# Optimization experiments

Measured on AMD Instinct MI355X. Metric: run time of the kernel, lower is better.

Reference implementation:

```python
import jax, jax.numpy as jnp
import numpy as np

S, B, C = 56, 32, 1024
T = 48
H = 1024          # hidden_size_decoder (== context_size C)
EMB = 512
RANK = 128
VOCAB = 32000


def setup_inputs() -> dict:
    key = jax.random.key(0)
    ks = jax.random.split(key, 16)
    w = 0.05
    inp = {
        "encoded": jax.random.normal(ks[0], (S, B, C), jnp.float32),
        "encoder_state": jax.random.normal(ks[1], (2, B, H), jnp.float32) * 0.1,
        "tgt_tokens": jax.random.randint(ks[2], (B, T), 0, VOCAB),
        "enc_lens": jax.random.randint(ks[3], (B,), S // 2, S + 1).astype(jnp.int32),
        "tgt_lens": jax.random.randint(ks[4], (B,), T // 2, T + 1).astype(jnp.int32),
        "E": jax.random.normal(ks[5], (VOCAB, RANK), jnp.float32) * w,
        "P": jax.random.normal(ks[6], (RANK, EMB), jnp.float32) * w,
        "W0": jax.random.normal(ks[7], (EMB + C, 4 * H), jnp.float32) * w,
        "U0": jax.random.normal(ks[8], (H, 4 * H), jnp.float32) * w,
        "b0": jnp.zeros((4 * H,), jnp.float32),
        "W1": jax.random.normal(ks[9], (H, 4 * H), jnp.float32) * w,
        "U1": jax.random.normal(ks[10], (H, 4 * H), jnp.float32) * w,
        "b1": jnp.zeros((4 * H,), jnp.float32),
        "Wo": jax.random.normal(ks[11], (H + C, EMB), jnp.float32) * w,
        "bo": jnp.zeros((EMB,), jnp.float32),
    }
    return inp


def _lstm_cell(x, h, c, W, U, b):
    gates = x @ W + h @ U + b                      # [B, 4H]
    i, f, g, o = jnp.split(gates, 4, axis=-1)      # torch LSTMCell gate order
    c_new = jax.nn.sigmoid(f) * c + jax.nn.sigmoid(i) * jnp.tanh(g)
    h_new = jax.nn.sigmoid(o) * jnp.tanh(c_new)
    return h_new, c_new


def reference(encoded, encoder_state, tgt_tokens, enc_lens, tgt_lens,
              E, P, W0, U0, b0, W1, U1, b1, Wo, bo):
    # encoded: [S, B, C] (padded encoder outputs), encoder_state: [L=2, B, H]
    enc_b = jnp.transpose(encoded, (1, 0, 2))                 # [B, S, C]
    enc_mask = jnp.arange(S)[None, :] >= enc_lens[:, None]    # [B, S] True = pad

    # factorized embedding lookup (dropout p=0)
    emb = (E[tgt_tokens] @ P)                                 # [B, T, EMB]
    emb_t = jnp.transpose(emb, (1, 0, 2))[: T - 1]            # [T-1, B, EMB]

    h0 = encoder_state                                        # [2, B, H]
    c0 = jnp.zeros_like(encoder_state)
    ctx0 = jnp.zeros((B, C), encoded.dtype)

    def step(carry, x_emb):
        h, c, ctx = carry
        x = jnp.concatenate([x_emb, ctx], axis=-1)            # [B, EMB+C]
        h0n, c0n = _lstm_cell(x, h[0], c[0], W0, U0, b0)
        h1n, c1n = _lstm_cell(h0n, h[1], c[1], W1, U1, b1)
        query = h1n                                           # no context projection
        scores = jnp.einsum("bsc,bc->bs", enc_b, query)       # [B, S]
        scores = jnp.where(enc_mask, -jnp.inf, scores)
        p_att = jax.nn.softmax(scores, axis=-1)
        ctx_new = jnp.einsum("bs,bsc->bc", p_att, enc_b)      # [B, C]
        return (jnp.stack([h0n, h1n]), jnp.stack([c0n, c1n]), ctx_new), (h1n, ctx_new)

    _, (decs, ctxs) = jax.lax.scan(step, (h0, c0, ctx0), emb_t)  # each [T-1, B, *]

    feats = jnp.concatenate([decs, ctxs], axis=-1)            # [T-1, B, H+C]
    hproj = jnp.tanh(feats @ Wo + bo)                          # [T-1, B, EMB]
    logits = (hproj @ P.T) @ E.T                               # [T-1, B, VOCAB]

    labels = tgt_tokens[:, 1:].T                               # [T-1, B]
    logp = jax.nn.log_softmax(logits, axis=-1)
    nll = -jnp.take_along_axis(logp, labels[..., None], axis=-1)[..., 0]
    valid = jnp.arange(T - 1)[:, None] < (tgt_lens[None, :] - 1)  # step t predicts token t+1
    loss = jnp.sum(jnp.where(valid, nll, 0.0))                 # CrossEntropyLoss(reduction='sum')
    return loss
```

## Files before the change

### kernel.cpp

```cpp
#include <hip/hip_runtime.h>
#include <math.h>

#define S_   56
#define B_   32
#define C_   1024
#define T_   48
#define TS   47
#define H_   1024
#define EMB_ 512
#define RANK_ 128
#define VOCAB_ 32000
#define G4   4096
#define NBLK 256

#define FL_DONE 8192
#define FL_P    8224
#define FL_SIZE 10496

using bf16x8 = __attribute__((ext_vector_type(8))) __bf16;
using f32x4  = __attribute__((ext_vector_type(4))) float;

__device__ __forceinline__ float sigmoidf_(float x){ return 1.0f/(1.0f+expf(-x)); }
__device__ __forceinline__ float b2f(__bf16 x){ return (float)x; }
__device__ __forceinline__ f32x4 z4(){ f32x4 z = {0.f,0.f,0.f,0.f}; return z; }

#define AG __HIP_MEMORY_SCOPE_AGENT
__device__ __forceinline__ void stc_u64(void* p, unsigned long long v){
  __hip_atomic_store((unsigned long long*)p, v, __ATOMIC_RELAXED, AG);
}

struct RedShared {
  float red[4][2][16][18];
};
struct AttnShared {
  union { float hS[1024]; float cred[7][64][8]; } u;
  float sS[64];
  float pS[64];
};
union alignas(16) SharedU { RedShared r; AttnShared a; };

__device__ __forceinline__ void bar_arrive(unsigned* bars, int bi, unsigned e){
  asm volatile("s_waitcnt vmcnt(0)" ::: "memory");
  __syncthreads();
  if (threadIdx.x == 0)
    __hip_atomic_store(bars + (size_t)bi*32, e, __ATOMIC_RELAXED, AG);
}
__device__ __forceinline__ void bar_wait_all(unsigned* bars, int bi, unsigned e){
  if (bi == 255){
    if (threadIdx.x < 256){
      while (__hip_atomic_load(bars + (size_t)threadIdx.x*32, __ATOMIC_RELAXED, AG) < e) {}
    }
    __syncthreads();
    if (threadIdx.x == 0)
      __hip_atomic_store(bars + FL_DONE, e, __ATOMIC_RELAXED, AG);
  } else {
    if (threadIdx.x == 0){
      while (__hip_atomic_load(bars + FL_DONE, __ATOMIC_RELAXED, AG) < e) {}
    }
    __syncthreads();
  }
  asm volatile("" ::: "memory");
}
__device__ __forceinline__ void bar_wait_direct(unsigned* bars, unsigned e){
  if (threadIdx.x < 256){
    while (__hip_atomic_load(bars + (size_t)threadIdx.x*32, __ATOMIC_RELAXED, AG) < e) {}
  }
  __syncthreads();
  asm volatile("" ::: "memory");
}
__device__ __forceinline__ void pflag_wait(unsigned* bars, unsigned t){
  if (threadIdx.x < 64){
    while (__hip_atomic_load(bars + FL_P + (size_t)threadIdx.x*32, __ATOMIC_RELAXED, AG) < t)
      __builtin_amdgcn_s_sleep(2);
  }
  __syncthreads();
  asm volatile("" ::: "memory");
}

__global__ void k_init(const float* __restrict__ es, __bf16* h0bm1, __bf16* fm1,
                       unsigned* bars){
  int i = blockIdx.x*blockDim.x + threadIdx.x;
  if (i < 32*H_){
    int b = i >> 10, j = i & 1023;
    h0bm1[(size_t)b*1024 + j]       = (__bf16)es[i];
    fm1[(size_t)b*2048 + j]         = (__bf16)es[32*H_ + i];
    fm1[(size_t)b*2048 + 1024 + j]  = (__bf16)0.0f;
  }
  if (i < FL_SIZE) bars[i] = 0u;
}

__global__ void k_cvt(const float* __restrict__ src, __bf16* __restrict__ dst, int n){
  int i = (blockIdx.x*blockDim.x + threadIdx.x)*4;
  if (i < n){
    float4 v = *(const float4*)(src + i);
    dst[i+0]=(__bf16)v.x; dst[i+1]=(__bf16)v.y; dst[i+2]=(__bf16)v.z; dst[i+3]=(__bf16)v.w;
  }
}

__global__ void k_embed(const float* __restrict__ E, const float* __restrict__ P,
                        const int* __restrict__ tok, __bf16* __restrict__ embb){
  int blk = blockIdx.x;
  int t = blk >> 5, b = blk & 31, tid = threadIdx.x;
  __shared__ float er[RANK_];
  int tk = tok[b*T_ + t];
  er[tid] = E[(size_t)tk*RANK_ + tid];
  __syncthreads();
  float4 acc = {0.f,0.f,0.f,0.f};
  int e = tid*4;
  for (int r2 = 0; r2 < RANK_; r2++){
    float ev = er[r2];
    float4 p = *(const float4*)(P + (size_t)r2*EMB_ + e);
    acc.x += ev*p.x; acc.y += ev*p.y; acc.z += ev*p.z; acc.w += ev*p.w;
  }
  size_t o = (size_t)blk*EMB_ + e;
  embb[o+0]=(__bf16)acc.x; embb[o+1]=(__bf16)acc.y;
  embb[o+2]=(__bf16)acc.z; embb[o+3]=(__bf16)acc.w;
}

__global__ void k_pack2(const float* __restrict__ W, int K1, const float* __restrict__ U,
                        __bf16* __restrict__ dst, int NCH){
  int ch = blockIdx.x;
  int g  = blockIdx.y >> 2;
  int band = blockIdx.y & 3;
  int tid = threadIdx.x;
  __shared__ __bf16 Tl[32][264];
  {
    int r = tid>>3, cs = tid&7;
    int kk = ch*32 + r;
    const float* src = (kk < K1) ? (W + (size_t)kk*G4 + g*1024 + band*256 + cs*32)
                                 : (U + (size_t)(kk-K1)*G4 + g*1024 + band*256 + cs*32);
    #pragma unroll
    for (int u=0;u<8;u++){
      float4 v = *(const float4*)(src + u*4);
      Tl[r][cs*32+u*4+0]=(__bf16)v.x; Tl[r][cs*32+u*4+1]=(__bf16)v.y;
      Tl[r][cs*32+u*4+2]=(__bf16)v.z; Tl[r][cs*32+u*4+3]=(__bf16)v.w;
    }
  }
  __syncthreads();
  int bil = tid>>2, aq = tid&3;
  int bi = band*64 + bil;
  #pragma unroll
  for (int q=0;q<4;q++){
    __bf16 o8[8];
    #pragma unroll
    for (int i=0;i<8;i++) o8[i] = Tl[aq*8+i][bil*4+q];
    int lane = aq*16 + g*4 + q;
    *(bf16x8*)(dst + (((size_t)bi*NCH + ch)*64 + lane)*8) = *(bf16x8*)o8;
  }
}

__global__ void k_packB(const float* __restrict__ src, __bf16* __restrict__ dst,
                        int K, int N, int tr){
  int kk0 = blockIdx.x*32, j0 = blockIdx.y*16, lane = threadIdx.x;
  int am = lane&15, aq = lane>>4;
  int j = j0 + am;
  __bf16 o8[8];
  #pragma unroll
  for (int i=0;i<8;i++){
    int k = kk0 + aq*8 + i;
    float v = tr ? src[(size_t)j*K + k] : src[(size_t)k*N + j];
    o8[i] = (__bf16)v;
  }
  int NCH = K/32, jt = j0>>4, ch = kk0>>5;
  *(bf16x8*)(dst + (((size_t)jt*NCH + ch)*64 + lane)*8) = *(bf16x8*)o8;
}

template<int NC>
__device__ __forceinline__ void accum(f32x4& acc0, f32x4& acc1,
    const __bf16* __restrict__ abase, int rs, const __bf16* wlds,
    int ch0, int am, int aq, int lane)
{
  const __bf16* a0p = abase + (size_t)am*rs + aq*8;
  const __bf16* a1p = abase + (size_t)(am+16)*rs + aq*8;
  const __bf16* wl  = wlds + (size_t)lane*8;
  #pragma unroll
  for (int c=0;c<NC;c++){
    int ch = ch0 + c;
    bf16x8 a0 = *(const bf16x8*)(a0p + (size_t)ch*32);
    bf16x8 a1 = *(const bf16x8*)(a1p + (size_t)ch*32);
    bf16x8 w  = *(const bf16x8*)(wl  + (size_t)ch*512);
    acc0 = __builtin_amdgcn_mfma_f32_16x16x32_bf16(a0, w, acc0, 0, 0, 0);
    acc1 = __builtin_amdgcn_mfma_f32_16x16x32_bf16(a1, w, acc1, 0, 0, 0);
  }
}

__device__ __forceinline__ void reduce_cell(SharedU& su, const f32x4& acc0, const f32x4& acc1,
    int bi, int tid, const float* __restrict__ bias, float& creg,
    __bf16* __restrict__ hout, int stride)
{
  int kw = tid>>6, lane = tid&63, am = lane&15, aq = lane>>4;
  if (kw >= 4){
    #pragma unroll
    for (int rg=0;rg<4;rg++){
      su.r.red[kw-4][0][aq*4+rg][am] = acc0[rg];
      su.r.red[kw-4][1][aq*4+rg][am] = acc1[rg];
    }
  }
  __syncthreads();
  if (kw < 4){
    #pragma unroll
    for (int rg=0;rg<4;rg++){
      su.r.red[kw][0][aq*4+rg][am] += acc0[rg];
      su.r.red[kw][1][aq*4+rg][am] += acc1[rg];
    }
  }
  __syncthreads();
  if (tid < 128){
    int b = tid>>2, q = tid&3;
    int mt = b>>4, r = b&15;
    float G0=0.f, G1=0.f, G2=0.f, G3=0.f;
    #pragma unroll
    for (int w2=0; w2<4; w2++){
      G0 += su.r.red[w2][mt][r][q];
      G1 += su.r.red[w2][mt][r][4+q];
      G2 += su.r.red[w2][mt][r][8+q];
      G3 += su.r.red[w2][mt][r][12+q];
    }
    int j = bi*4 + q;
    float gi = G0 + bias[j];
    float gf = G1 + bias[1024 + j];
    float gg = G2 + bias[2048 + j];
    float go = G3 + bias[3072 + j];
    float ii = sigmoidf_(gi), ff = sigmoidf_(gf), gv = tanhf(gg), oo = sigmoidf_(go);
    float cv = ff*creg + ii*gv;
    float hv = oo*tanhf(cv);
    creg = cv;
    union { __bf16 h; unsigned short s; } hu; hu.h = (__bf16)hv;
    unsigned h0v = hu.s;
    unsigned h1v = __shfl_down(h0v, 1);
    unsigned h2v = __shfl_down(h0v, 2);
    unsigned h3v = __shfl_down(h0v, 3);
    if (q == 0){
      unsigned long long pk = (unsigned long long)(h0v & 0xffffu)
                            | ((unsigned long long)(h1v & 0xffffu) << 16)
                            | ((unsigned long long)(h2v & 0xffffu) << 32)
                            | ((unsigned long long)(h3v & 0xffffu) << 48);
      stc_u64(hout + (size_t)b*stride + bi*4, pk);
    }
  }
}

__device__ __forceinline__ void attn_block(AttnShared& sa, int b, int chalf, int tid,
    const __bf16* __restrict__ encb, const int* __restrict__ enc_lens,
    __bf16* __restrict__ fbt)
{
  if (tid < 128){
    bf16x8 h8 = *(const bf16x8*)(fbt + (size_t)b*2048 + tid*8);
    #pragma unroll
    for (int u=0;u<8;u++) sa.u.hS[tid*8+u] = b2f(h8[u]);
  }
  __syncthreads();
  int w = tid >> 6, lane = tid & 63;
  for (int s = w; s < S_; s += 8){
    const __bf16* er = encb + ((size_t)s*32 + b)*C_;
    float a = 0.f;
    #pragma unroll
    for (int half = 0; half < 2; half++){
      int k = lane*8 + half*512;
      bf16x8 e8 = *(const bf16x8*)(er + k);
      #pragma unroll
      for (int u=0;u<8;u++) a += b2f(e8[u]) * sa.u.hS[k+u];
    }
    #pragma unroll
    for (int off=32; off>0; off>>=1) a += __shfl_down(a, off);
    if (lane == 0) sa.sS[s] = a;
  }
  __syncthreads();
  if (tid < 64){
    int len = enc_lens[b];
    float sc = (tid < len && tid < S_) ? sa.sS[tid] : -1e30f;
    float m = sc;
    #pragma unroll
    for (int off=32; off>0; off>>=1) m = fmaxf(m, __shfl_xor(m, off));
    float e = expf(sc - m);
    float ssum = e;
    #pragma unroll
    for (int off=32; off>0; off>>=1) ssum += __shfl_xor(ssum, off);
    sa.pS[tid] = e / ssum;
  }
  __syncthreads();
  int cg = tid & 63, sg = tid >> 6;
  float a8[8];
  #pragma unroll
  for (int i=0;i<8;i++) a8[i] = 0.f;
  for (int s = sg; s < S_; s += 8){
    float p = sa.pS[s];
    bf16x8 e8 = *(const bf16x8*)(encb + ((size_t)s*32 + b)*C_ + chalf*512 + cg*8);
    #pragma unroll
    for (int i=0;i<8;i++) a8[i] += p * b2f(e8[i]);
  }
  if (sg > 0){
    #pragma unroll
    for (int i=0;i<8;i++) sa.u.cred[sg-1][cg][i] = a8[i];
  }
  __syncthreads();
  if (sg == 0){
    union { __bf16 bb[8]; unsigned long long u[2]; } cu;
    #pragma unroll
    for (int i=0;i<8;i++){
      float v = a8[i];
      #pragma unroll
      for (int k=0;k<7;k++) v += sa.u.cred[k][cg][i];
      cu.bb[i] = (__bf16)v;
    }
    stc_u64(fbt + (size_t)b*2048 + 1024 + chalf*512 + cg*8,     cu.u[0]);
    stc_u64(fbt + (size_t)b*2048 + 1024 + chalf*512 + cg*8 + 4, cu.u[1]);
  }
}

__global__ __launch_bounds__(512) void k_loop(
    const __bf16* __restrict__ WP0, const __bf16* __restrict__ WP1,
    const float* __restrict__ b0, const float* __restrict__ b1,
    __bf16* __restrict__ h0b,
    __bf16* __restrict__ featsb,
    const __bf16* __restrict__ embb,
    const __bf16* __restrict__ encb, const int* __restrict__ enc_lens,
    unsigned* bars)
{
  __shared__ __bf16 wB0[80*512];
  __shared__ __bf16 wB1[64*512];
  __shared__ SharedU su;
  int bi = blockIdx.x, tid = threadIdx.x;
  int kw = tid>>6, lane = tid&63, am = lane&15, aq = lane>>4;

  {
    const bf16x8* g0 = (const bf16x8*)(WP0 + (size_t)bi*80*512);
    const bf16x8* g1 = (const bf16x8*)(WP1 + (size_t)bi*64*512);
    bf16x8* l0 = (bf16x8*)wB0;
    bf16x8* l1 = (bf16x8*)wB1;
    for (int idx = tid; idx < 80*64; idx += 512) l0[idx] = g0[idx];
    for (int idx = tid; idx < 64*64; idx += 512) l1[idx] = g1[idx];
  }
  __syncthreads();

  float c0r = 0.f, c1r = 0.f;
  f32x4 g00 = z4(), g01 = z4(), g10 = z4(), g11 = z4();

  accum<2>(g00, g01, embb,                 512,  wB0, kw*2,    am, aq, lane);
  accum<4>(g00, g01, h0b - 32768 - 1536,   1024, wB0, 48+kw*4, am, aq, lane);

  unsigned e = 0;
  for (int t = 0; t < TS; t++){
    const __bf16* fprev = featsb + ((size_t)(t-1))*65536;
    __bf16* h0t = h0b + (size_t)t*32768;
    __bf16* ft  = featsb + (size_t)t*65536;

    pflag_wait(bars, (unsigned)t);
    accum<4>(g00, g01, fprev + 512, 2048, wB0, 16+kw*4, am, aq, lane);
    reduce_cell(su, g00, g01, bi, tid, b0, c0r, h0t, 1024);
    g00 = z4(); g01 = z4();
    bar_arrive(bars, bi, ++e);
    accum<4>(g10, g11, fprev - 1024, 2048, wB1, 32+kw*4, am, aq, lane);
    bar_wait_all(bars, bi, e);

    accum<4>(g10, g11, h0t, 1024, wB1, kw*4, am, aq, lane);
    reduce_cell(su, g10, g11, bi, tid, b1, c1r, ft, 2048);
    g10 = z4(); g11 = z4();
    bar_arrive(bars, bi, ++e);
    if (t + 1 < TS){
      accum<2>(g00, g01, embb + (size_t)(t+1)*16384, 512,  wB0, kw*2,    am, aq, lane);
      accum<4>(g00, g01, h0t - 1536,                 1024, wB0, 48+kw*4, am, aq, lane);
    }

    if (bi < 64){
      bar_wait_direct(bars, e);
      attn_block(su.a, bi & 31, bi >> 5, tid, encb, enc_lens, ft);
      asm volatile("s_waitcnt vmcnt(0)" ::: "memory");
      __syncthreads();
      if (tid == 0)
        __hip_atomic_store(bars + FL_P + (size_t)bi*32, (unsigned)(t+1), __ATOMIC_RELAXED, AG);
    }
  }
}

__global__ __launch_bounds__(256) void k_hproj_mfma(
    const __bf16* __restrict__ fb, const __bf16* __restrict__ WoP,
    const float* __restrict__ bo, __bf16* __restrict__ hpb)
{
  int nt = blockIdx.x, jb = blockIdx.y, tid = threadIdx.x;
  int w = tid>>6, lane = tid&63;
  int mt = w&1, jw = w>>1;
  int am = lane&15, aq = lane>>4;
  const __bf16* aRow = fb + ((size_t)(nt*32 + mt*16 + am))*2048 + aq*8;
  int jt = jb*2 + jw;
  const __bf16* bptr = WoP + ((size_t)jt*64)*512 + lane*8;
  f32x4 acc = {0,0,0,0};
  bf16x8 ar0 = *(const bf16x8*)(aRow);
  bf16x8 br0 = *(const bf16x8*)(bptr);
  bf16x8 ar1 = *(const bf16x8*)(aRow + 32);
  bf16x8 br1 = *(const bf16x8*)(bptr + 512);
  for (int ch = 0; ch < 64; ch += 2){
    bf16x8 a0 = ar0, b0 = br0, a1 = ar1, b1 = br1;
    if (ch + 2 < 64){
      ar0 = *(const bf16x8*)(aRow + (ch+2)*32);
      br0 = *(const bf16x8*)(bptr + (size_t)(ch+2)*512);
      ar1 = *(const bf16x8*)(aRow + (ch+3)*32);
      br1 = *(const bf16x8*)(bptr + (size_t)(ch+3)*512);
    }
    acc = __builtin_amdgcn_mfma_f32_16x16x32_bf16(a0, b0, acc, 0, 0, 0);
    acc = __builtin_amdgcn_mfma_f32_16x16x32_bf16(a1, b1, acc, 0, 0, 0);
  }
  int jcol = jb*32 + jw*16 + am;
  float bv = bo[jcol];
  #pragma unroll
  for (int rg=0; rg<4; rg++){
    int m = nt*32 + mt*16 + aq*4 + rg;
    hpb[(size_t)m*512 + jcol] = (__bf16)tanhf(acc[rg] + bv);
  }
}

__global__ __launch_bounds__(256) void k_rproj_mfma(
    const __bf16* __restrict__ hpb, const __bf16* __restrict__ PP,
    __bf16* __restrict__ rb)
{
  int nt = blockIdx.x, jb = blockIdx.y, tid = threadIdx.x;
  int w = tid>>6, lane = tid&63;
  int mt = w&1, jw = w>>1;
  int am = lane&15, aq = lane>>4;
  const __bf16* aRow = hpb + ((size_t)(nt*32 + mt*16 + am))*512 + aq*8;
  int jt = jb*2 + jw;
  const __bf16* bptr = PP + ((size_t)jt*16)*512 + lane*8;
  f32x4 acc = {0,0,0,0};
  #pragma unroll
  for (int ch = 0; ch < 16; ch++){
    bf16x8 a = *(const bf16x8*)(aRow + ch*32);
    bf16x8 b = *(const bf16x8*)(bptr + (size_t)ch*512);
    acc = __builtin_amdgcn_mfma_f32_16x16x32_bf16(a, b, acc, 0, 0, 0);
  }
  int jcol = jb*32 + jw*16 + am;
  #pragma unroll
  for (int rg=0; rg<4; rg++){
    int m = nt*32 + mt*16 + aq*4 + rg;
    rb[(size_t)m*RANK_ + jcol] = (__bf16)acc[rg];
  }
}

__global__ __launch_bounds__(256) void k_vocab2(
    const __bf16* __restrict__ rb, const __bf16* __restrict__ Eb,
    const int* __restrict__ tok,
    float* __restrict__ mpart, float* __restrict__ lpart,
    float* __restrict__ lablog)
{
  int vc = blockIdx.x, tid = threadIdx.x;
  int w = tid>>6, lane = tid&63;
  int am = lane&15, aq = lane>>4;
  int vb = vc*128 + w*32;
  bf16x8 bfr[2][4];
  #pragma unroll
  for (int vt=0; vt<2; vt++)
    #pragma unroll
    for (int ks=0; ks<4; ks++)
      bfr[vt][ks] = *(const bf16x8*)(Eb + ((size_t)(vb + vt*16 + am))*RANK_ + ks*32 + aq*8);

  __shared__ float redM[4][32], redL[4][32];
  for (int nt = 0; nt < TS; nt++){
    f32x4 acc[2][2] = {{{0,0,0,0},{0,0,0,0}},{{0,0,0,0},{0,0,0,0}}};
    #pragma unroll
    for (int mt=0; mt<2; mt++){
      #pragma unroll
      for (int ks=0; ks<4; ks++){
        bf16x8 a = *(const bf16x8*)(rb + ((size_t)(nt*32 + mt*16 + am))*RANK_ + ks*32 + aq*8);
        acc[mt][0] = __builtin_amdgcn_mfma_f32_16x16x32_bf16(a, bfr[0][ks], acc[mt][0], 0,0,0);
        acc[mt][1] = __builtin_amdgcn_mfma_f32_16x16x32_bf16(a, bfr[1][ks], acc[mt][1], 0,0,0);
      }
    }
    #pragma unroll
    for (int mt=0; mt<2; mt++){
      #pragma unroll
      for (int rg=0; rg<4; rg++){
        int row = mt*16 + aq*4 + rg;
        int n = nt*32 + row;
        int lbl = tok[row*T_ + nt + 1];
        float v0 = acc[mt][0][rg], v1 = acc[mt][1][rg];
        if (vb + am == lbl)      lablog[n] = v0;
        if (vb + 16 + am == lbl) lablog[n] = v1;
        float m = fmaxf(v0, v1);
        #pragma unroll
        for (int off=1; off<16; off<<=1) m = fmaxf(m, __shfl_xor(m, off));
        float l = expf(v0 - m) + expf(v1 - m);
        #pragma unroll
        for (int off=1; off<16; off<<=1) l += __shfl_xor(l, off);
        if (am == 0){ redM[w][row] = m; redL[w][row] = l; }
      }
    }
    __syncthreads();
    if (tid < 32){
      float M = fmaxf(fmaxf(redM[0][tid], redM[1][tid]), fmaxf(redM[2][tid], redM[3][tid]));
      float L = 0.f;
      #pragma unroll
      for (int ww=0; ww<4; ww++) L += redL[ww][tid]*expf(redM[ww][tid] - M);
      mpart[(size_t)(nt*32 + tid)*250 + vc] = M;
      lpart[(size_t)(nt*32 + tid)*250 + vc] = L;
    }
    __syncthreads();
  }
}

__global__ void k_loss1(const float* __restrict__ mpart, const float* __restrict__ lpart,
                        const float* __restrict__ lablog, const int* __restrict__ tgt_lens,
                        float* __restrict__ tpart){
  int t = blockIdx.x, tid = threadIdx.x;
  int row = tid >> 3, cq = tid & 7;
  int n = t*32 + row;
  float m = -1e30f;
  for (int c = cq; c < 250; c += 8) m = fmaxf(m, mpart[(size_t)n*250 + c]);
  #pragma unroll
  for (int off=1; off<8; off<<=1) m = fmaxf(m, __shfl_xor(m, off));
  float l = 0.f;
  for (int c = cq; c < 250; c += 8) l += lpart[(size_t)n*250 + c]*expf(mpart[(size_t)n*250 + c] - m);
  #pragma unroll
  for (int off=1; off<8; off<<=1) l += __shfl_xor(l, off);
  __shared__ float red[32];
  if (cq == 0)
    red[row] = (t < tgt_lens[row] - 1) ? (m + logf(l) - lablog[n]) : 0.f;
  __syncthreads();
  if (tid == 0){
    float s = 0.f;
    #pragma unroll
    for (int i=0;i<32;i++) s += red[i];
    tpart[t] = s;
  }
}

__global__ void k_loss2(const float* __restrict__ tpart, float* __restrict__ out){
  int tid = threadIdx.x;
  float v = (tid < TS) ? tpart[tid] : 0.f;
  #pragma unroll
  for (int off=32; off>0; off>>=1) v += __shfl_down(v, off);
  if (tid == 0) out[0] = v;
}

extern "C" void kernel_launch(void* const* d_in, const int* in_sizes, int n_in,
                              void* d_out, int out_size, void* d_ws, size_t ws_size,
                              hipStream_t stream){
  const float* enc      = (const float*)d_in[0];
  const float* es       = (const float*)d_in[1];
  const int*   tok      = (const int*)  d_in[2];
  const int*   enc_lens = (const int*)  d_in[3];
  const int*   tgt_lens = (const int*)  d_in[4];
  const float* E        = (const float*)d_in[5];
  const float* P        = (const float*)d_in[6];
  const float* W0       = (const float*)d_in[7];
  const float* U0       = (const float*)d_in[8];
  const float* b0       = (const float*)d_in[9];
  const float* W1       = (const float*)d_in[10];
  const float* U1       = (const float*)d_in[11];
  const float* b1       = (const float*)d_in[12];
  const float* Wo       = (const float*)d_in[13];
  const float* bo       = (const float*)d_in[14];
  float* out = (float*)d_out;

  float* fb = (float*)d_ws;
  size_t fo = 0;
  float* mpart = fb + fo; fo += (size_t)TS*32*250;
  float* lpart = fb + fo; fo += (size_t)TS*32*250;
  float* lab   = fb + fo; fo += (size_t)TS*32;
  float* tpart = fb + fo; fo += 64;
  unsigned* bars = (unsigned*)(fb + fo); fo += FL_SIZE;
  __bf16* bb = (__bf16*)(fb + fo);
  size_t bo2 = 0;
  __bf16* WP0    = bb + bo2; bo2 += (size_t)4096*2560;
  __bf16* WP1    = bb + bo2; bo2 += (size_t)4096*2048;
  __bf16* encb   = bb + bo2; bo2 += (size_t)S_*32*C_;
  __bf16* embb   = bb + bo2; bo2 += (size_t)TS*32*EMB_;
  __bf16* rbuf   = bb + bo2; bo2 += (size_t)TS*32*RANK_;
  __bf16* WoP    = bb + bo2; bo2 += (size_t)2048*512;
  __bf16* PP     = bb + bo2; bo2 += (size_t)512*128;
  __bf16* featsb0= bb + bo2; bo2 += (size_t)(TS+1)*32*2048;
  __bf16* hpb    = bb + bo2; bo2 += (size_t)TS*32*EMB_;
  __bf16* h0b0   = bb + bo2; bo2 += (size_t)(TS+1)*32*1024;
  __bf16* Eb     = WP0;

  __bf16* featsb = featsb0 + (size_t)32*2048;
  __bf16* h0b    = h0b0 + (size_t)32*1024;

  k_init<<<128, 256, 0, stream>>>(es, h0b0, featsb0, bars);
  k_cvt<<<(S_*32*C_/4 + 255)/256, 256, 0, stream>>>(enc, encb, S_*32*C_);
  k_embed<<<TS*32, 128, 0, stream>>>(E, P, tok, embb);
  k_pack2<<<dim3(80,16), 256, 0, stream>>>(W0, 1536, U0, WP0, 80);
  k_pack2<<<dim3(64,16), 256, 0, stream>>>(W1, 1024, U1, WP1, 64);
  k_packB<<<dim3(64,32), 64, 0, stream>>>(Wo, WoP, 2048, 512, 0);
  k_packB<<<dim3(16,8), 64, 0, stream>>>(P, PP, 512, 128, 1);

  k_loop<<<NBLK, 512, 0, stream>>>(WP0, WP1, b0, b1, h0b, featsb,
                                   embb, encb, enc_lens, bars);

  k_cvt<<<(VOCAB_*RANK_/4 + 255)/256, 256, 0, stream>>>(E, Eb, VOCAB_*RANK_);

  k_hproj_mfma<<<dim3(TS,16), 256, 0, stream>>>(featsb, WoP, bo, hpb);
  k_rproj_mfma<<<dim3(TS,4), 256, 0, stream>>>(hpb, PP, rbuf);
  k_vocab2<<<250, 256, 0, stream>>>(rbuf, Eb, tok, mpart, lpart, lab);
  k_loss1<<<TS, 256, 0, stream>>>(mpart, lpart, lab, tgt_lens, tpart);
  k_loss2<<<1, 64, 0, stream>>>(tpart, out);
}
```

Measured before the change: 1.392 ms.

## Fuse preprocessing into one kernel and post-loop stages into persistent loop

```diff
diff --git a/kernel.cpp b/kernel.cpp
--- a/kernel.cpp
+++ b/kernel.cpp
@@ -28,6 +28,12 @@
 __device__ __forceinline__ void stc_u64(void* p, unsigned long long v){
   __hip_atomic_store((unsigned long long*)p, v, __ATOMIC_RELAXED, AG);
 }
+__device__ __forceinline__ void stc_f32(float* p, float v){
+  __hip_atomic_store(p, v, __ATOMIC_RELAXED, AG);
+}
+__device__ __forceinline__ float ldc_f32(const float* p){
+  return __hip_atomic_load(p, __ATOMIC_RELAXED, AG);
+}
 
 struct RedShared {
   float red[4][2][16][18];
@@ -37,7 +43,12 @@
   float sS[64];
   float pS[64];
 };
-union alignas(16) SharedU { RedShared r; AttnShared a; };
+struct VocShared {
+  float redM[4][32];
+  float redL[4][32];
+  float red1[32];
+};
+union alignas(16) SharedU { RedShared r; AttnShared a; VocShared v; };
 
 __device__ __forceinline__ void bar_arrive(unsigned* bars, int bi, unsigned e){
   asm volatile("s_waitcnt vmcnt(0)" ::: "memory");
@@ -71,98 +82,122 @@
 __device__ __forceinline__ void pflag_wait(unsigned* bars, unsigned t){
   if (threadIdx.x < 64){
     while (__hip_atomic_load(bars + FL_P + (size_t)threadIdx.x*32, __ATOMIC_RELAXED, AG) < t)
-      __builtin_amdgcn_s_sleep(2);
+      __builtin_amdgcn_s_sleep(1);
   }
   __syncthreads();
   asm volatile("" ::: "memory");
 }
 
-__global__ void k_init(const float* __restrict__ es, __bf16* h0bm1, __bf16* fm1,
-                       unsigned* bars){
-  int i = blockIdx.x*blockDim.x + threadIdx.x;
-  if (i < 32*H_){
-    int b = i >> 10, j = i & 1023;
-    h0bm1[(size_t)b*1024 + j]       = (__bf16)es[i];
-    fm1[(size_t)b*2048 + j]         = (__bf16)es[32*H_ + i];
-    fm1[(size_t)b*2048 + 1024 + j]  = (__bf16)0.0f;
-  }
-  if (i < FL_SIZE) bars[i] = 0u;
-}
-
-__global__ void k_cvt(const float* __restrict__ src, __bf16* __restrict__ dst, int n){
-  int i = (blockIdx.x*blockDim.x + threadIdx.x)*4;
-  if (i < n){
-    float4 v = *(const float4*)(src + i);
-    dst[i+0]=(__bf16)v.x; dst[i+1]=(__bf16)v.y; dst[i+2]=(__bf16)v.z; dst[i+3]=(__bf16)v.w;
-  }
-}
-
-__global__ void k_embed(const float* __restrict__ E, const float* __restrict__ P,
-                        const int* __restrict__ tok, __bf16* __restrict__ embb){
-  int blk = blockIdx.x;
-  int t = blk >> 5, b = blk & 31, tid = threadIdx.x;
-  __shared__ float er[RANK_];
-  int tk = tok[b*T_ + t];
-  er[tid] = E[(size_t)tk*RANK_ + tid];
-  __syncthreads();
-  float4 acc = {0.f,0.f,0.f,0.f};
-  int e = tid*4;
-  for (int r2 = 0; r2 < RANK_; r2++){
-    float ev = er[r2];
-    float4 p = *(const float4*)(P + (size_t)r2*EMB_ + e);
-    acc.x += ev*p.x; acc.y += ev*p.y; acc.z += ev*p.z; acc.w += ev*p.w;
-  }
-  size_t o = (size_t)blk*EMB_ + e;
-  embb[o+0]=(__bf16)acc.x; embb[o+1]=(__bf16)acc.y;
-  embb[o+2]=(__bf16)acc.z; embb[o+3]=(__bf16)acc.w;
-}
-
-__global__ void k_pack2(const float* __restrict__ W, int K1, const float* __restrict__ U,
-                        __bf16* __restrict__ dst, int NCH){
-  int ch = blockIdx.x;
-  int g  = blockIdx.y >> 2;
-  int band = blockIdx.y & 3;
-  int tid = threadIdx.x;
-  __shared__ __bf16 Tl[32][264];
-  {
-    int r = tid>>3, cs = tid&7;
-    int kk = ch*32 + r;
-    const float* src = (kk < K1) ? (W + (size_t)kk*G4 + g*1024 + band*256 + cs*32)
-                                 : (U + (size_t)(kk-K1)*G4 + g*1024 + band*256 + cs*32);
-    #pragma unroll
-    for (int u=0;u<8;u++){
-      float4 v = *(const float4*)(src + u*4);
-      Tl[r][cs*32+u*4+0]=(__bf16)v.x; Tl[r][cs*32+u*4+1]=(__bf16)v.y;
-      Tl[r][cs*32+u*4+2]=(__bf16)v.z; Tl[r][cs*32+u*4+3]=(__bf16)v.w;
-    }
-  }
-  __syncthreads();
-  int bil = tid>>2, aq = tid&3;
-  int bi = band*64 + bil;
-  #pragma unroll
-  for (int q=0;q<4;q++){
+__global__ __launch_bounds__(256) void k_pre(
+    const float* __restrict__ W0, const float* __restrict__ U0,
+    const float* __restrict__ W1, const float* __restrict__ U1,
+    const float* __restrict__ Wo, const float* __restrict__ P,
+    const float* __restrict__ E,  const float* __restrict__ enc,
+    const float* __restrict__ es, const int* __restrict__ tok,
+    __bf16* __restrict__ WP0, __bf16* __restrict__ WP1,
+    __bf16* __restrict__ WoP, __bf16* __restrict__ PP,
+    __bf16* __restrict__ Eb,  __bf16* __restrict__ encb,
+    __bf16* __restrict__ embb, __bf16* __restrict__ h0bm1,
+    __bf16* __restrict__ fm1, unsigned* __restrict__ bars)
+{
+  __shared__ union { __bf16 Tl[32][264]; float er[RANK_]; } sp;
+  int id = blockIdx.x, tid = threadIdx.x;
+
+  if (id < 2304){
+    const float* A; const float* Bs; __bf16* dst; int K1, NCH, p;
+    if (id < 1280){ p = id;        A = W0; Bs = U0; dst = WP0; K1 = 1536; NCH = 80; }
+    else          { p = id - 1280; A = W1; Bs = U1; dst = WP1; K1 = 1024; NCH = 64; }
+    int ch = (NCH==80) ? (p % 80) : (p % 64);
+    int gy = (NCH==80) ? (p / 80) : (p / 64);
+    int g = gy >> 2, band = gy & 3;
+    {
+      int r = tid>>3, cs = tid&7;
+      int kk = ch*32 + r;
+      const float* src = (kk < K1) ? (A + (size_t)kk*G4 + g*1024 + band*256 + cs*32)
+                                   : (Bs + (size_t)(kk-K1)*G4 + g*1024 + band*256 + cs*32);
+      #pragma unroll
+      for (int u=0;u<8;u++){
+        float4 v = *(const float4*)(src + u*4);
+        sp.Tl[r][cs*32+u*4+0]=(__bf16)v.x; sp.Tl[r][cs*32+u*4+1]=(__bf16)v.y;
+        sp.Tl[r][cs*32+u*4+2]=(__bf16)v.z; sp.Tl[r][cs*32+u*4+3]=(__bf16)v.w;
+      }
+    }
+    __syncthreads();
+    int bil = tid>>2, aq = tid&3;
+    int bi = band*64 + bil;
+    #pragma unroll
+    for (int q=0;q<4;q++){
+      __bf16 o8[8];
+      #pragma unroll
+      for (int i=0;i<8;i++) o8[i] = sp.Tl[aq*8+i][bil*4+q];
+      int lane = aq*16 + g*4 + q;
+      *(bf16x8*)(dst + (((size_t)bi*NCH + ch)*64 + lane)*8) = *(bf16x8*)o8;
+    }
+  } else if (id < 2848){
+    int sub = tid>>6, lane = tid&63;
+    int am = lane&15, aq = lane>>4;
+    const float* src; __bf16* dst; int K, N, tr, unit;
+    if (id < 2816){ unit = (id-2304)*4 + sub; src = Wo; dst = WoP; K = 2048; N = 512; tr = 0; }
+    else          { unit = (id-2816)*4 + sub; src = P;  dst = PP;  K = 512;  N = 128; tr = 1; }
+    int nbx = K/32;
+    int bx = unit % nbx, by = unit / nbx;
+    int kk0 = bx*32, j0 = by*16;
+    int j = j0 + am;
     __bf16 o8[8];
     #pragma unroll
-    for (int i=0;i<8;i++) o8[i] = Tl[aq*8+i][bil*4+q];
-    int lane = aq*16 + g*4 + q;
-    *(bf16x8*)(dst + (((size_t)bi*NCH + ch)*64 + lane)*8) = *(bf16x8*)o8;
-  }
-}
-
-__global__ void k_packB(const float* __restrict__ src, __bf16* __restrict__ dst,
-                        int K, int N, int tr){
-  int kk0 = blockIdx.x*32, j0 = blockIdx.y*16, lane = threadIdx.x;
-  int am = lane&15, aq = lane>>4;
-  int j = j0 + am;
-  __bf16 o8[8];
-  #pragma unroll
-  for (int i=0;i<8;i++){
-    int k = kk0 + aq*8 + i;
-    float v = tr ? src[(size_t)j*K + k] : src[(size_t)k*N + j];
-    o8[i] = (__bf16)v;
-  }
-  int NCH = K/32, jt = j0>>4, ch = kk0>>5;
-  *(bf16x8*)(dst + (((size_t)jt*NCH + ch)*64 + lane)*8) = *(bf16x8*)o8;
+    for (int i=0;i<8;i++){
+      int k = kk0 + aq*8 + i;
+      float v = tr ? src[(size_t)j*K + k] : src[(size_t)k*N + j];
+      o8[i] = (__bf16)v;
+    }
+    int NCH = K/32, jt = j0>>4, ch = kk0>>5;
+    *(bf16x8*)(dst + (((size_t)jt*NCH + ch)*64 + lane)*8) = *(bf16x8*)o8;
+  } else if (id < 4352){
+    int blk = id - 2848;
+    int t = blk >> 5, b = blk & 31;
+    int tk = tok[b*T_ + t];
+    if (tid < 128) sp.er[tid] = E[(size_t)tk*RANK_ + tid];
+    __syncthreads();
+    if (tid < 128){
+      float4 acc = {0.f,0.f,0.f,0.f};
+      int e = tid*4;
+      for (int r2 = 0; r2 < RANK_; r2++){
+        float ev = sp.er[r2];
+        float4 p = *(const float4*)(P + (size_t)r2*EMB_ + e);
+        acc.x += ev*p.x; acc.y += ev*p.y; acc.z += ev*p.z; acc.w += ev*p.w;
+      }
+      size_t o = (size_t)blk*EMB_ + e;
+      embb[o+0]=(__bf16)acc.x; embb[o+1]=(__bf16)acc.y;
+      embb[o+2]=(__bf16)acc.z; embb[o+3]=(__bf16)acc.w;
+    }
+  } else {
+    const unsigned NE = 458752u;
+    const unsigned NEB = 1024000u;
+    const unsigned NI = 32768u;
+    const unsigned NF = FL_SIZE;
+    unsigned u0 = (unsigned)(id - 4352)*256u + (unsigned)tid;
+    for (unsigned u = u0; u < NE+NEB+NI+NF; u += 2048u*256u){
+      if (u < NE){
+        int i4 = u*4;
+        float4 v = *(const float4*)(enc + i4);
+        encb[i4+0]=(__bf16)v.x; encb[i4+1]=(__bf16)v.y;
+        encb[i4+2]=(__bf16)v.z; encb[i4+3]=(__bf16)v.w;
+      } else if (u < NE+NEB){
+        int i4 = (u-NE)*4;
+        float4 v = *(const float4*)(E + i4);
+        Eb[i4+0]=(__bf16)v.x; Eb[i4+1]=(__bf16)v.y;
+        Eb[i4+2]=(__bf16)v.z; Eb[i4+3]=(__bf16)v.w;
+      } else if (u < NE+NEB+NI){
+        unsigned i = u - NE - NEB;
+        int b = i >> 10, j = i & 1023;
+        h0bm1[(size_t)b*1024 + j]       = (__bf16)es[i];
+        fm1[(size_t)b*2048 + j]         = (__bf16)es[32*H_ + i];
+        fm1[(size_t)b*2048 + 1024 + j]  = (__bf16)0.0f;
+      } else {
+        bars[u - NE - NEB - NI] = 0u;
+      }
+    }
+  }
 }
 
 template<int NC>
@@ -308,14 +343,185 @@
   }
 }
 
+__device__ __forceinline__ void hproj_tile(int nt, int jq, int tid,
+    const __bf16* __restrict__ fb, const __bf16* __restrict__ WoP,
+    const float* __restrict__ bo, __bf16* __restrict__ hpb)
+{
+  int w = tid>>6, lane = tid&63;
+  int mt = w&1, jw = w>>1;
+  int am = lane&15, aq = lane>>4;
+  int jt = jq*4 + jw;
+  const __bf16* aRow = fb + ((size_t)(nt*32 + mt*16 + am))*2048 + aq*8;
+  const __bf16* bptr = WoP + ((size_t)jt*64)*512 + lane*8;
+  f32x4 acc = {0,0,0,0};
+  for (int ch = 0; ch < 64; ch++){
+    bf16x8 a = *(const bf16x8*)(aRow + ch*32);
+    bf16x8 b = *(const bf16x8*)(bptr + (size_t)ch*512);
+    acc = __builtin_amdgcn_mfma_f32_16x16x32_bf16(a, b, acc, 0, 0, 0);
+  }
+  int jcol = jt*16 + am;
+  float bv = bo[jcol];
+  #pragma unroll
+  for (int rg=0; rg<4; rg++){
+    int m = nt*32 + mt*16 + aq*4 + rg;
+    union { __bf16 h; unsigned short s; } hu; hu.h = (__bf16)tanhf(acc[rg] + bv);
+    unsigned v0 = hu.s;
+    unsigned v1 = __shfl_down(v0,1);
+    unsigned v2 = __shfl_down(v0,2);
+    unsigned v3 = __shfl_down(v0,3);
+    if ((am&3)==0){
+      unsigned long long pk = (unsigned long long)(v0&0xffffu)
+        | ((unsigned long long)(v1&0xffffu)<<16)
+        | ((unsigned long long)(v2&0xffffu)<<32)
+        | ((unsigned long long)(v3&0xffffu)<<48);
+      stc_u64(hpb + (size_t)m*512 + jcol, pk);
+    }
+  }
+}
+
+__device__ __forceinline__ void rproj_tile(int nt, int half, int tid,
+    const __bf16* __restrict__ hpb, const __bf16* __restrict__ PP,
+    __bf16* __restrict__ rb)
+{
+  int w = tid>>6, lane = tid&63;
+  int jb = half*2 + (w>>2);
+  int mt = w&1, jw = (w>>1)&1;
+  int am = lane&15, aq = lane>>4;
+  int jt = jb*2 + jw;
+  const __bf16* aRow = hpb + ((size_t)(nt*32 + mt*16 + am))*512 + aq*8;
+  const __bf16* bptr = PP + ((size_t)jt*16)*512 + lane*8;
+  f32x4 acc = {0,0,0,0};
+  #pragma unroll
+  for (int ch = 0; ch < 16; ch++){
+    bf16x8 a = *(const bf16x8*)(aRow + ch*32);
+    bf16x8 b = *(const bf16x8*)(bptr + (size_t)ch*512);
+    acc = __builtin_amdgcn_mfma_f32_16x16x32_bf16(a, b, acc, 0, 0, 0);
+  }
+  int jcol = jt*16 + am;
+  #pragma unroll
+  for (int rg=0; rg<4; rg++){
+    int m = nt*32 + mt*16 + aq*4 + rg;
+    union { __bf16 h; unsigned short s; } hu; hu.h = (__bf16)acc[rg];
+    unsigned v0 = hu.s;
+    unsigned v1 = __shfl_down(v0,1);
+    unsigned v2 = __shfl_down(v0,2);
+    unsigned v3 = __shfl_down(v0,3);
+    if ((am&3)==0){
+      unsigned long long pk = (unsigned long long)(v0&0xffffu)
+        | ((unsigned long long)(v1&0xffffu)<<16)
+        | ((unsigned long long)(v2&0xffffu)<<32)
+        | ((unsigned long long)(v3&0xffffu)<<48);
+      stc_u64(rb + (size_t)m*RANK_ + jcol, pk);
+    }
+  }
+}
+
+__device__ __forceinline__ void vocab_chunk(SharedU& su, int vc, int tid,
+    const __bf16* __restrict__ rb, const __bf16* __restrict__ Eb,
+    const int* __restrict__ tok,
+    float* __restrict__ mpart, float* __restrict__ lpart,
+    float* __restrict__ lablog)
+{
+  int w = tid>>6, lane = tid&63;
+  int am = lane&15, aq = lane>>4;
+  int vb = vc*128 + w*32;
+  bf16x8 bfr[2][4];
+  if (tid < 256){
+    #pragma unroll
+    for (int vt=0; vt<2; vt++)
+      #pragma unroll
+      for (int ks=0; ks<4; ks++)
+        bfr[vt][ks] = *(const bf16x8*)(Eb + ((size_t)(vb + vt*16 + am))*RANK_ + ks*32 + aq*8);
+  }
+  for (int nt = 0; nt < TS; nt++){
+    if (tid < 256){
+      f32x4 acc[2][2] = {{{0,0,0,0},{0,0,0,0}},{{0,0,0,0},{0,0,0,0}}};
+      #pragma unroll
+      for (int mt=0; mt<2; mt++){
+        #pragma unroll
+        for (int ks=0; ks<4; ks++){
+          bf16x8 a = *(const bf16x8*)(rb + ((size_t)(nt*32 + mt*16 + am))*RANK_ + ks*32 + aq*8);
+          acc[mt][0] = __builtin_amdgcn_mfma_f32_16x16x32_bf16(a, bfr[0][ks], acc[mt][0], 0,0,0);
+          acc[mt][1] = __builtin_amdgcn_mfma_f32_16x16x32_bf16(a, bfr[1][ks], acc[mt][1], 0,0,0);
+        }
+      }
+      #pragma unroll
+      for (int mt=0; mt<2; mt++){
+        #pragma unroll
+        for (int rg=0; rg<4; rg++){
+          int row = mt*16 + aq*4 + rg;
+          int n = nt*32 + row;
+          int lbl = tok[row*T_ + nt + 1];
+          float v0 = acc[mt][0][rg], v1 = acc[mt][1][rg];
+          if (vb + am == lbl)      stc_f32(lablog + n, v0);
+          if (vb + 16 + am == lbl) stc_f32(lablog + n, v1);
+          float m = fmaxf(v0, v1);
+          #pragma unroll
+          for (int off=1; off<16; off<<=1) m = fmaxf(m, __shfl_xor(m, off));
+          float l = expf(v0 - m) + expf(v1 - m);
+          #pragma unroll
+          for (int off=1; off<16; off<<=1) l += __shfl_xor(l, off);
+          if (am == 0){ su.v.redM[w][row] = m; su.v.redL[w][row] = l; }
+        }
+      }
+    }
+    __syncthreads();
+    if (tid < 32){
+      float M = fmaxf(fmaxf(su.v.redM[0][tid], su.v.redM[1][tid]),
+                      fmaxf(su.v.redM[2][tid], su.v.redM[3][tid]));
+      float L = 0.f;
+      #pragma unroll
+      for (int ww=0; ww<4; ww++) L += su.v.redL[ww][tid]*expf(su.v.redM[ww][tid] - M);
+      stc_f32(mpart + (size_t)(nt*32 + tid)*250 + vc, M);
+      stc_f32(lpart + (size_t)(nt*32 + tid)*250 + vc, L);
+    }
+    __syncthreads();
+  }
+}
+
+__device__ __forceinline__ void loss1_block(SharedU& su, int t, int tid,
+    const float* __restrict__ mpart, const float* __restrict__ lpart,
+    const float* __restrict__ lablog, const int* __restrict__ tgt_lens,
+    float* __restrict__ tpart)
+{
+  if (tid < 256){
+    int row = tid >> 3, cq = tid & 7;
+    int n = t*32 + row;
+    float m = -1e30f;
+    for (int c = cq; c < 250; c += 8) m = fmaxf(m, ldc_f32(mpart + (size_t)n*250 + c));
+    #pragma unroll
+    for (int off=1; off<8; off<<=1) m = fmaxf(m, __shfl_xor(m, off));
+    float l = 0.f;
+    for (int c = cq; c < 250; c += 8)
+      l += ldc_f32(lpart + (size_t)n*250 + c)*expf(ldc_f32(mpart + (size_t)n*250 + c) - m);
+    #pragma unroll
+    for (int off=1; off<8; off<<=1) l += __shfl_xor(l, off);
+    if (cq == 0)
+      su.v.red1[row] = (t < tgt_lens[row] - 1) ? (m + logf(l) - ldc_f32(lablog + n)) : 0.f;
+  }
+  __syncthreads();
+  if (tid == 0){
+    float s = 0.f;
+    #pragma unroll
+    for (int i=0;i<32;i++) s += su.v.red1[i];
+    stc_f32(tpart + t, s);
+  }
+}
+
 __global__ __launch_bounds__(512) void k_loop(
     const __bf16* __restrict__ WP0, const __bf16* __restrict__ WP1,
     const float* __restrict__ b0, const float* __restrict__ b1,
-    __bf16* __restrict__ h0b,
-    __bf16* __restrict__ featsb,
+    __bf16* __restrict__ h0b, __bf16* __restrict__ featsb,
     const __bf16* __restrict__ embb,
     const __bf16* __restrict__ encb, const int* __restrict__ enc_lens,
-    unsigned* bars)
+    unsigned* bars,
+    const __bf16* __restrict__ WoP, const float* __restrict__ bo,
+    const __bf16* __restrict__ PP, const __bf16* __restrict__ Eb,
+    const int* __restrict__ tok, const int* __restrict__ tgt_lens,
+    __bf16* __restrict__ hpb, __bf16* __restrict__ rbuf,
+    float* __restrict__ mpart, float* __restrict__ lpart,
+    float* __restrict__ lab, float* __restrict__ tpart,
+    float* __restrict__ out)
 {
   __shared__ __bf16 wB0[80*512];
   __shared__ __bf16 wB1[64*512];
@@ -371,163 +577,35 @@
         __hip_atomic_store(bars + FL_P + (size_t)bi*32, (unsigned)(t+1), __ATOMIC_RELAXED, AG);
     }
   }
-}
-
-__global__ __launch_bounds__(256) void k_hproj_mfma(
-    const __bf16* __restrict__ fb, const __bf16* __restrict__ WoP,
-    const float* __restrict__ bo, __bf16* __restrict__ hpb)
-{
-  int nt = blockIdx.x, jb = blockIdx.y, tid = threadIdx.x;
-  int w = tid>>6, lane = tid&63;
-  int mt = w&1, jw = w>>1;
-  int am = lane&15, aq = lane>>4;
-  const __bf16* aRow = fb + ((size_t)(nt*32 + mt*16 + am))*2048 + aq*8;
-  int jt = jb*2 + jw;
-  const __bf16* bptr = WoP + ((size_t)jt*64)*512 + lane*8;
-  f32x4 acc = {0,0,0,0};
-  bf16x8 ar0 = *(const bf16x8*)(aRow);
-  bf16x8 br0 = *(const bf16x8*)(bptr);
-  bf16x8 ar1 = *(const bf16x8*)(aRow + 32);
-  bf16x8 br1 = *(const bf16x8*)(bptr + 512);
-  for (int ch = 0; ch < 64; ch += 2){
-    bf16x8 a0 = ar0, b0 = br0, a1 = ar1, b1 = br1;
-    if (ch + 2 < 64){
-      ar0 = *(const bf16x8*)(aRow + (ch+2)*32);
-      br0 = *(const bf16x8*)(bptr + (size_t)(ch+2)*512);
-      ar1 = *(const bf16x8*)(aRow + (ch+3)*32);
-      br1 = *(const bf16x8*)(bptr + (size_t)(ch+3)*512);
-    }
-    acc = __builtin_amdgcn_mfma_f32_16x16x32_bf16(a0, b0, acc, 0, 0, 0);
-    acc = __builtin_amdgcn_mfma_f32_16x16x32_bf16(a1, b1, acc, 0, 0, 0);
-  }
-  int jcol = jb*32 + jw*16 + am;
-  float bv = bo[jcol];
-  #pragma unroll
-  for (int rg=0; rg<4; rg++){
-    int m = nt*32 + mt*16 + aq*4 + rg;
-    hpb[(size_t)m*512 + jcol] = (__bf16)tanhf(acc[rg] + bv);
-  }
-}
-
-__global__ __launch_bounds__(256) void k_rproj_mfma(
-    const __bf16* __restrict__ hpb, const __bf16* __restrict__ PP,
-    __bf16* __restrict__ rb)
-{
-  int nt = blockIdx.x, jb = blockIdx.y, tid = threadIdx.x;
-  int w = tid>>6, lane = tid&63;
-  int mt = w&1, jw = w>>1;
-  int am = lane&15, aq = lane>>4;
-  const __bf16* aRow = hpb + ((size_t)(nt*32 + mt*16 + am))*512 + aq*8;
-  int jt = jb*2 + jw;
-  const __bf16* bptr = PP + ((size_t)jt*16)*512 + lane*8;
-  f32x4 acc = {0,0,0,0};
-  #pragma unroll
-  for (int ch = 0; ch < 16; ch++){
-    bf16x8 a = *(const bf16x8*)(aRow + ch*32);
-    bf16x8 b = *(const bf16x8*)(bptr + (size_t)ch*512);
-    acc = __builtin_amdgcn_mfma_f32_16x16x32_bf16(a, b, acc, 0, 0, 0);
-  }
-  int jcol = jb*32 + jw*16 + am;
-  #pragma unroll
-  for (int rg=0; rg<4; rg++){
-    int m = nt*32 + mt*16 + aq*4 + rg;
-    rb[(size_t)m*RANK_ + jcol] = (__bf16)acc[rg];
-  }
-}
-
-__global__ __launch_bounds__(256) void k_vocab2(
-    const __bf16* __restrict__ rb, const __bf16* __restrict__ Eb,
-    const int* __restrict__ tok,
-    float* __restrict__ mpart, float* __restrict__ lpart,
-    float* __restrict__ lablog)
-{
-  int vc = blockIdx.x, tid = threadIdx.x;
-  int w = tid>>6, lane = tid&63;
-  int am = lane&15, aq = lane>>4;
-  int vb = vc*128 + w*32;
-  bf16x8 bfr[2][4];
-  #pragma unroll
-  for (int vt=0; vt<2; vt++)
-    #pragma unroll
-    for (int ks=0; ks<4; ks++)
-      bfr[vt][ks] = *(const bf16x8*)(Eb + ((size_t)(vb + vt*16 + am))*RANK_ + ks*32 + aq*8);
-
-  __shared__ float redM[4][32], redL[4][32];
-  for (int nt = 0; nt < TS; nt++){
-    f32x4 acc[2][2] = {{{0,0,0,0},{0,0,0,0}},{{0,0,0,0},{0,0,0,0}}};
-    #pragma unroll
-    for (int mt=0; mt<2; mt++){
-      #pragma unroll
-      for (int ks=0; ks<4; ks++){
-        bf16x8 a = *(const bf16x8*)(rb + ((size_t)(nt*32 + mt*16 + am))*RANK_ + ks*32 + aq*8);
-        acc[mt][0] = __builtin_amdgcn_mfma_f32_16x16x32_bf16(a, bfr[0][ks], acc[mt][0], 0,0,0);
-        acc[mt][1] = __builtin_amdgcn_mfma_f32_16x16x32_bf16(a, bfr[1][ks], acc[mt][1], 0,0,0);
-      }
-    }
-    #pragma unroll
-    for (int mt=0; mt<2; mt++){
-      #pragma unroll
-      for (int rg=0; rg<4; rg++){
-        int row = mt*16 + aq*4 + rg;
-        int n = nt*32 + row;
-        int lbl = tok[row*T_ + nt + 1];
-        float v0 = acc[mt][0][rg], v1 = acc[mt][1][rg];
-        if (vb + am == lbl)      lablog[n] = v0;
-        if (vb + 16 + am == lbl) lablog[n] = v1;
-        float m = fmaxf(v0, v1);
-        #pragma unroll
-        for (int off=1; off<16; off<<=1) m = fmaxf(m, __shfl_xor(m, off));
-        float l = expf(v0 - m) + expf(v1 - m);
-        #pragma unroll
-        for (int off=1; off<16; off<<=1) l += __shfl_xor(l, off);
-        if (am == 0){ redM[w][row] = m; redL[w][row] = l; }
-      }
-    }
-    __syncthreads();
-    if (tid < 32){
-      float M = fmaxf(fmaxf(redM[0][tid], redM[1][tid]), fmaxf(redM[2][tid], redM[3][tid]));
-      float L = 0.f;
-      #pragma unroll
-      for (int ww=0; ww<4; ww++) L += redL[ww][tid]*expf(redM[ww][tid] - M);
-      mpart[(size_t)(nt*32 + tid)*250 + vc] = M;
-      lpart[(size_t)(nt*32 + tid)*250 + vc] = L;
-    }
-    __syncthreads();
-  }
-}
-
-__global__ void k_loss1(const float* __restrict__ mpart, const float* __restrict__ lpart,
-                        const float* __restrict__ lablog, const int* __restrict__ tgt_lens,
-                        float* __restrict__ tpart){
-  int t = blockIdx.x, tid = threadIdx.x;
-  int row = tid >> 3, cq = tid & 7;
-  int n = t*32 + row;
-  float m = -1e30f;
-  for (int c = cq; c < 250; c += 8) m = fmaxf(m, mpart[(size_t)n*250 + c]);
-  #pragma unroll
-  for (int off=1; off<8; off<<=1) m = fmaxf(m, __shfl_xor(m, off));
-  float l = 0.f;
-  for (int c = cq; c < 250; c += 8) l += lpart[(size_t)n*250 + c]*expf(mpart[(size_t)n*250 + c] - m);
-  #pragma unroll
-  for (int off=1; off<8; off<<=1) l += __shfl_xor(l, off);
-  __shared__ float red[32];
-  if (cq == 0)
-    red[row] = (t < tgt_lens[row] - 1) ? (m + logf(l) - lablog[n]) : 0.f;
-  __syncthreads();
-  if (tid == 0){
-    float s = 0.f;
-    #pragma unroll
-    for (int i=0;i<32;i++) s += red[i];
-    tpart[t] = s;
-  }
-}
-
-__global__ void k_loss2(const float* __restrict__ tpart, float* __restrict__ out){
-  int tid = threadIdx.x;
-  float v = (tid < TS) ? tpart[tid] : 0.f;
-  #pragma unroll
-  for (int off=32; off>0; off>>=1) v += __shfl_down(v, off);
-  if (tid == 0) out[0] = v;
+
+  pflag_wait(bars, (unsigned)TS);
+
+  for (int tau = bi; tau < 376; tau += 256)
+    hproj_tile(tau >> 3, tau & 7, tid, featsb, WoP, bo, hpb);
+  bar_arrive(bars, bi, ++e);
+  bar_wait_all(bars, bi, e);
+
+  if (bi < 94)
+    rproj_tile(bi >> 1, bi & 1, tid, hpb, PP, rbuf);
+  bar_arrive(bars, bi, ++e);
+  bar_wait_all(bars, bi, e);
+
+  if (bi < 250)
+    vocab_chunk(su, bi, tid, rbuf, Eb, tok, mpart, lpart, lab);
+  bar_arrive(bars, bi, ++e);
+  bar_wait_all(bars, bi, e);
+
+  if (bi < 47)
+    loss1_block(su, bi, tid, mpart, lpart, lab, tgt_lens, tpart);
+  bar_arrive(bars, bi, ++e);
+  bar_wait_all(bars, bi, e);
+
+  if (bi == 0 && tid < 64){
+    float v = (tid < TS) ? ldc_f32(tpart + tid) : 0.f;
+    #pragma unroll
+    for (int off=32; off>0; off>>=1) v += __shfl_down(v, off);
+    if (tid == 0) out[0] = v;
+  }
 }
 
 extern "C" void kernel_launch(void* const* d_in, const int* in_sizes, int n_in,
@@ -552,15 +630,11 @@
 
   float* fb = (float*)d_ws;
   size_t fo = 0;
-  float* mpart = fb + fo; fo += (size_t)TS*32*250;
-  float* lpart = fb + fo; fo += (size_t)TS*32*250;
-  float* lab   = fb + fo; fo += (size_t)TS*32;
-  float* tpart = fb + fo; fo += 64;
   unsigned* bars = (unsigned*)(fb + fo); fo += FL_SIZE;
   __bf16* bb = (__bf16*)(fb + fo);
   size_t bo2 = 0;
-  __bf16* WP0    = bb + bo2; bo2 += (size_t)4096*2560;
-  __bf16* WP1    = bb + bo2; bo2 += (size_t)4096*2048;
+  __bf16* WP0    = bb + bo2; bo2 += (size_t)256*80*512;
+  __bf16* WP1    = bb + bo2; bo2 += (size_t)256*64*512;
   __bf16* encb   = bb + bo2; bo2 += (size_t)S_*32*C_;
   __bf16* embb   = bb + bo2; bo2 += (size_t)TS*32*EMB_;
   __bf16* rbuf   = bb + bo2; bo2 += (size_t)TS*32*RANK_;
@@ -569,27 +643,22 @@
   __bf16* featsb0= bb + bo2; bo2 += (size_t)(TS+1)*32*2048;
   __bf16* hpb    = bb + bo2; bo2 += (size_t)TS*32*EMB_;
   __bf16* h0b0   = bb + bo2; bo2 += (size_t)(TS+1)*32*1024;
-  __bf16* Eb     = WP0;
+  __bf16* Eb     = bb + bo2; bo2 += (size_t)VOCAB_*RANK_;
 
   __bf16* featsb = featsb0 + (size_t)32*2048;
   __bf16* h0b    = h0b0 + (size_t)32*1024;
 
-  k_init<<<128, 256, 0, stream>>>(es, h0b0, featsb0, bars);
-  k_cvt<<<(S_*32*C_/4 + 255)/256, 256, 0, stream>>>(enc, encb, S_*32*C_);
-  k_embed<<<TS*32, 128, 0, stream>>>(E, P, tok, embb);
-  k_pack2<<<dim3(80,16), 256, 0, stream>>>(W0, 1536, U0, WP0, 80);
-  k_pack2<<<dim3(64,16), 256, 0, stream>>>(W1, 1024, U1, WP1, 64);
-  k_packB<<<dim3(64,32), 64, 0, stream>>>(Wo, WoP, 2048, 512, 0);
-  k_packB<<<dim3(16,8), 64, 0, stream>>>(P, PP, 512, 128, 1);
+  float* mpart = (float*)featsb0;
+  float* lpart = mpart + (size_t)TS*32*250;
+  float* lab   = lpart + (size_t)TS*32*250;
+  float* tpart = lab + (size_t)TS*32;
+
+  k_pre<<<6400, 256, 0, stream>>>(W0, U0, W1, U1, Wo, P, E, enc, es, tok,
+                                  WP0, WP1, WoP, PP, Eb, encb, embb,
+                                  h0b0, featsb0, bars);
 
   k_loop<<<NBLK, 512, 0, stream>>>(WP0, WP1, b0, b1, h0b, featsb,
-                                   embb, encb, enc_lens, bars);
-
-  k_cvt<<<(VOCAB_*RANK_/4 + 255)/256, 256, 0, stream>>>(E, Eb, VOCAB_*RANK_);
-
-  k_hproj_mfma<<<dim3(TS,16), 256, 0, stream>>>(featsb, WoP, bo, hpb);
-  k_rproj_mfma<<<dim3(TS,4), 256, 0, stream>>>(hpb, PP, rbuf);
-  k_vocab2<<<250, 256, 0, stream>>>(rbuf, Eb, tok, mpart, lpart, lab);
-  k_loss1<<<TS, 256, 0, stream>>>(mpart, lpart, lab, tgt_lens, tpart);
-  k_loss2<<<1, 64, 0, stream>>>(tpart, out);
-}
+                                   embb, encb, enc_lens, bars,
+                                   WoP, bo, PP, Eb, tok, tgt_lens,
+                                   hpb, rbuf, mpart, lpart, lab, tpart, out);
+}
```

Measured after the change: 1.396 ms. About the same (+0.3%).
